# Kernel optimization log

Hardware: AMD Instinct MI355X
Metric: run time of the kernel (lower is better)

## Reference

```python
import jax, jax.numpy as jnp
import numpy as np

T = 8192
F = 128   # feature_size
H = 2048  # hidden_size
PRED_LEN = 12  # pred_length (fc_out head exists in module but is unused in forward)


def setup_inputs() -> dict:
    key = jax.random.key(0)
    ks = jax.random.split(key, 10)
    s_ih = 1.0 / np.sqrt(H)
    inp = {
        "x": jax.random.normal(ks[0], (T, F), dtype=jnp.float32),
        # PyTorch nn.LSTM params, gate order [i, f, g, o]
        "W_ih": jax.random.uniform(ks[1], (4 * H, F), jnp.float32, -s_ih, s_ih),
        "W_hh": jax.random.uniform(ks[2], (4 * H, H), jnp.float32, -s_ih, s_ih),
        "b_ih": jax.random.uniform(ks[3], (4 * H,), jnp.float32, -s_ih, s_ih),
        "b_hh": jax.random.uniform(ks[4], (4 * H,), jnp.float32, -s_ih, s_ih),
        # self.linear: Linear(H, H)
        "W_lin": jax.random.uniform(ks[5], (H, H), jnp.float32, -s_ih, s_ih),
        "b_lin": jax.random.uniform(ks[6], (H,), jnp.float32, -s_ih, s_ih),
        # self.one_out: Linear(H, 2)
        "W_out": jax.random.uniform(ks[7], (2, H), jnp.float32, -s_ih, s_ih),
        "b_out": jax.random.uniform(ks[8], (2,), jnp.float32, -s_ih, s_ih),
    }
    return inp


def _lstm_last_h(x, W_ih, W_hh, b_ih, b_hh):
    # x: [T, F]; returns final hidden state h: [H]
    # Precompute input projections for all timesteps: [T, 4H]
    x_proj = x @ W_ih.T + (b_ih + b_hh)

    def step(carry, xp):
        h, c = carry
        gates = xp + h @ W_hh.T  # [4H]
        i = jax.nn.sigmoid(gates[0 * H:1 * H])
        f = jax.nn.sigmoid(gates[1 * H:2 * H])
        g = jnp.tanh(gates[2 * H:3 * H])
        o = jax.nn.sigmoid(gates[3 * H:4 * H])
        c = f * c + i * g
        h = o * jnp.tanh(c)
        return (h, c), None

    h0 = jnp.zeros((H,), x.dtype)
    c0 = jnp.zeros((H,), x.dtype)
    (h, _), _ = jax.lax.scan(step, (h0, c0), x_proj)
    return h


def reference(x, W_ih, W_hh, b_ih, b_hh, W_lin, b_lin, W_out, b_out):
    h = _lstm_last_h(x, W_ih, W_hh, b_ih, b_hh)        # [H]
    y = h @ W_lin.T + b_lin                            # [H]
    y = y @ W_out.T + b_out                            # [2]
    return y.reshape(1, 1, 2)                          # matches torch (1,1,2)
```

## Files before the change

### kernel.cpp

```cpp
#include <hip/hip_runtime.h>


#define H      2048
#define TSTEPS 8192
#define FEAT   128
#define NBLK   256
#define NTHR   512

typedef float vf4 __attribute__((ext_vector_type(4)));
typedef float vf2 __attribute__((ext_vector_type(2)));
typedef unsigned long long u64;
typedef unsigned int u32;

__device__ __forceinline__ float sigm(float xv) {
  return __builtin_amdgcn_rcpf(1.0f + __expf(-xv));
}
__device__ __forceinline__ float tanh_(float xv) {
  return 1.0f - 2.0f * __builtin_amdgcn_rcpf(__expf(2.0f * xv) + 1.0f);
}

__device__ __forceinline__ u64 aload64(const u64* p) {
  return __hip_atomic_load(p, __ATOMIC_RELAXED, __HIP_MEMORY_SCOPE_AGENT);
}
__device__ __forceinline__ u32 aload32(const u32* p) {
  return __hip_atomic_load(p, __ATOMIC_RELAXED, __HIP_MEMORY_SCOPE_AGENT);
}
__device__ __forceinline__ void astoreu(u32* p, u32 v) {
  __hip_atomic_store(p, v, __ATOMIC_RELAXED, __HIP_MEMORY_SCOPE_AGENT);
}
__device__ __forceinline__ void astore64(u64* p, u64 v) {
  __hip_atomic_store(p, v, __ATOMIC_RELAXED, __HIP_MEMORY_SCOPE_AGENT);
}
__device__ __forceinline__ int  tag_of(u64 d) { return (int)(u32)(d >> 32); }
__device__ __forceinline__ float val_of(u64 d) { return __uint_as_float((u32)d); }
__device__ __forceinline__ u64  pack(int tag, float v) {
  return ((u64)(u32)tag << 32) | (u64)__float_as_uint(v);
}

#define DECLG(g) vf4 w##g##_0, w##g##_1, w##g##_2, w##g##_3, \
                     w##g##_4, w##g##_5, w##g##_6, w##g##_7; \
                 vf2 wih##g; float bias##g; float acc##g;

#define LOADG(g) { \
  const int row_ = (g) * H + j; \
  const float* wr_ = W_hh + (long)row_ * H; \
  w##g##_0 = *(const vf4*)(wr_ + 4*(ln      )); \
  w##g##_1 = *(const vf4*)(wr_ + 4*(ln +  64)); \
  w##g##_2 = *(const vf4*)(wr_ + 4*(ln + 128)); \
  w##g##_3 = *(const vf4*)(wr_ + 4*(ln + 192)); \
  w##g##_4 = *(const vf4*)(wr_ + 4*(ln + 256)); \
  w##g##_5 = *(const vf4*)(wr_ + 4*(ln + 320)); \
  w##g##_6 = *(const vf4*)(wr_ + 4*(ln + 384)); \
  w##g##_7 = *(const vf4*)(wr_ + 4*(ln + 448)); \
  wih##g  = *(const vf2*)(W_ih + (long)row_ * FEAT + 2*ln); \
  bias##g = b_ih[row_] + b_hh[row_]; }

#define PIN(g) asm volatile("" : \
  "+v"(w##g##_0), "+v"(w##g##_1), "+v"(w##g##_2), "+v"(w##g##_3), \
  "+v"(w##g##_4), "+v"(w##g##_5), "+v"(w##g##_6), "+v"(w##g##_7), \
  "+v"(wih##g), "+v"(bias##g));

#define LDSREAD(k, ldsrow) \
  const vf4 hv##k = *(const vf4*)&(ldsrow)[4*(ln + 64*(k))];

#define FMA_G(g, c) \
  acc##g = __builtin_fmaf(w##g##_##c.x, h4_.x, acc##g); \
  acc##g = __builtin_fmaf(w##g##_##c.y, h4_.y, acc##g); \
  acc##g = __builtin_fmaf(w##g##_##c.z, h4_.z, acc##g); \
  acc##g = __builtin_fmaf(w##g##_##c.w, h4_.w, acc##g);

#define FMA_C(c) { const vf4 h4_ = hv##c; \
  FMA_G(0, c) FMA_G(1, c) FMA_G(2, c) FMA_G(3, c) }

#define REDUCE(g) { float a_ = acc##g; \
  a_ += __shfl_xor(a_, 1);  a_ += __shfl_xor(a_, 2);  a_ += __shfl_xor(a_, 4); \
  a_ += __shfl_xor(a_, 8);  a_ += __shfl_xor(a_, 16); a_ += __shfl_xor(a_, 32); \
  acc##g = a_ + bias##g; }

__device__ __forceinline__ void poll_and_stage(const u32* __restrict__ slots,
                                               const u64* __restrict__ hq_par,
                                               int tgt,
                                               float* __restrict__ ldsrow,
                                               int wv, int ln) {
  const int base = wv * 256 + 4 * ln;
  const u64* hp = hq_par + base;
  u64 d0 = aload64(hp + 0);
  u64 d1 = aload64(hp + 1);
  u64 d2 = aload64(hp + 2);
  u64 d3 = aload64(hp + 3);

  const u32* sp = slots + wv * 32 + (ln & 31);
  const bool act = (ln < 32);
  int v0 = act ? (int)aload32(sp) : 0x7fffffff;
  int v1 = act ? (int)aload32(sp) : 0x7fffffff;
  int v2 = act ? (int)aload32(sp) : 0x7fffffff;
  while (!__all(v0 >= tgt)) {
    __builtin_amdgcn_s_sleep(1);
    v0 = v1;
    v1 = v2;
    v2 = (act && v1 < tgt) ? (int)aload32(sp) : v1;
  }
  while (!__all((tag_of(d0) >= tgt) & (tag_of(d1) >= tgt) &
                (tag_of(d2) >= tgt) & (tag_of(d3) >= tgt))) {
    if (tag_of(d0) < tgt) d0 = aload64(hp + 0);
    if (tag_of(d1) < tgt) d1 = aload64(hp + 1);
    if (tag_of(d2) < tgt) d2 = aload64(hp + 2);
    if (tag_of(d3) < tgt) d3 = aload64(hp + 3);
  }
  vf4 hv;
  hv.x = val_of(d0);
  hv.y = val_of(d1);
  hv.z = val_of(d2);
  hv.w = val_of(d3);
  *(vf4*)&ldsrow[base] = hv;
}

__global__ __launch_bounds__(NTHR, 2)
void lstm_persist(const float* __restrict__ x,
                  const float* __restrict__ W_ih,
                  const float* __restrict__ W_hh,
                  const float* __restrict__ b_ih,
                  const float* __restrict__ b_hh,
                  const float* __restrict__ W_lin,
                  const float* __restrict__ b_lin,
                  const float* __restrict__ W_out,
                  const float* __restrict__ b_out,
                  float* __restrict__ out,
                  float* __restrict__ ws)
{
  const int tid = threadIdx.x;
  const int b   = blockIdx.x;
  const int wv  = tid >> 6;
  const int ln  = tid & 63;

  u64* hq    = (u64*)ws;
  u32* slots = (u32*)(ws + 4 * H);

  __shared__ __align__(16) float h_lds[2][H];

  *(vf4*)&h_lds[0][4 * tid] = (vf4)(0.0f);

  const int j = b * 8 + wv;
  DECLG(0) DECLG(1) DECLG(2) DECLG(3)
  LOADG(0) LOADG(1) LOADG(2) LOADG(3)
  PIN(0) PIN(1) PIN(2) PIN(3)

  __syncthreads();

  float cst = 0.0f;

  #pragma unroll 1
  for (int t = 0; t < TSTEPS; ++t) {
    const vf2 xr = *(const vf2*)(x + (long)t * FEAT + 2 * ln);
    float* ldsrow = h_lds[t & 1];

    if (t > 0)
      poll_and_stage(slots, hq + (t & 1) * H, t, ldsrow, wv, ln);
    __syncthreads();

    LDSREAD(0, ldsrow) LDSREAD(1, ldsrow) LDSREAD(2, ldsrow) LDSREAD(3, ldsrow)
    LDSREAD(4, ldsrow) LDSREAD(5, ldsrow) LDSREAD(6, ldsrow) LDSREAD(7, ldsrow)

    acc0 = wih0.x * xr.x + wih0.y * xr.y;
    acc1 = wih1.x * xr.x + wih1.y * xr.y;
    acc2 = wih2.x * xr.x + wih2.y * xr.y;
    acc3 = wih3.x * xr.x + wih3.y * xr.y;

    FMA_C(0) FMA_C(1) FMA_C(2) FMA_C(3)
    FMA_C(4) FMA_C(5) FMA_C(6) FMA_C(7)

    REDUCE(0) REDUCE(1) REDUCE(2) REDUCE(3)

    const float iv = sigm(acc0);
    const float fv = sigm(acc1);
    const float gv = tanh_(acc2);
    const float ov = sigm(acc3);
    cst = fv * cst + iv * gv;
    const float hval = ov * tanh_(cst);

    if (ln == 0)
      astore64(hq + ((t + 1) & 1) * H + j, pack(t + 1, hval));
    __syncthreads();
    if (tid == 0)
      astoreu(slots + b, (u32)(t + 1));
  }

  {
    float* ldsrow = h_lds[0];
    poll_and_stage(slots, hq, TSTEPS, ldsrow, wv, ln);
    __syncthreads();

    float a0 = 0.0f;
    const float* wl = W_lin + (long)j * H;
    #pragma unroll
    for (int k = 0; k < 8; ++k) {
      const vf4 h4 = *(const vf4*)&ldsrow[4 * (ln + 64 * k)];
      const vf4 u  = *(const vf4*)(wl + 4 * (ln + 64 * k));
      a0 += u.x * h4.x + u.y * h4.y + u.z * h4.z + u.w * h4.w;
    }
    a0 += __shfl_xor(a0, 1);  a0 += __shfl_xor(a0, 2);  a0 += __shfl_xor(a0, 4);
    a0 += __shfl_xor(a0, 8);  a0 += __shfl_xor(a0, 16); a0 += __shfl_xor(a0, 32);

    if (ln == 0)
      astore64(hq + H + j, pack(TSTEPS + 1, a0 + b_lin[j]));
    __syncthreads();
    if (tid == 0)
      astoreu(slots + b, (u32)(TSTEPS + 1));
  }

  if (b == 0 && wv == 0) {
    const u32* sp = slots + 4 * ln;
    int v0 = (int)aload32(sp + 0), v1 = (int)aload32(sp + 1);
    int v2 = (int)aload32(sp + 2), v3 = (int)aload32(sp + 3);
    const int tgt = TSTEPS + 1;
    while (!__all((v0 >= tgt) & (v1 >= tgt) & (v2 >= tgt) & (v3 >= tgt))) {
      __builtin_amdgcn_s_sleep(1);
      if (v0 < tgt) v0 = (int)aload32(sp + 0);
      if (v1 < tgt) v1 = (int)aload32(sp + 1);
      if (v2 < tgt) v2 = (int)aload32(sp + 2);
      if (v3 < tgt) v3 = (int)aload32(sp + 3);
    }
    float p0 = 0.0f, p1 = 0.0f;
    #pragma unroll
    for (int k = 0; k < 32; ++k) {
      const u64 d  = aload64(hq + H + ln + 64 * k);
      const float y = val_of(d);
      const int c  = ln + 64 * k;
      p0 = __builtin_fmaf(W_out[c],     y, p0);
      p1 = __builtin_fmaf(W_out[H + c], y, p1);
    }
    p0 += __shfl_xor(p0, 1);  p0 += __shfl_xor(p0, 2);  p0 += __shfl_xor(p0, 4);
    p0 += __shfl_xor(p0, 8);  p0 += __shfl_xor(p0, 16); p0 += __shfl_xor(p0, 32);
    p1 += __shfl_xor(p1, 1);  p1 += __shfl_xor(p1, 2);  p1 += __shfl_xor(p1, 4);
    p1 += __shfl_xor(p1, 8);  p1 += __shfl_xor(p1, 16); p1 += __shfl_xor(p1, 32);
    if (ln == 0) {
      out[0] = p0 + b_out[0];
      out[1] = p1 + b_out[1];
    }
  }
}

extern "C" void kernel_launch(void* const* d_in, const int* in_sizes, int n_in,
                              void* d_out, int out_size, void* d_ws, size_t ws_size,
                              hipStream_t stream) {
  const float* x     = (const float*)d_in[0];
  const float* W_ih  = (const float*)d_in[1];
  const float* W_hh  = (const float*)d_in[2];
  const float* b_ih  = (const float*)d_in[3];
  const float* b_hh  = (const float*)d_in[4];
  const float* W_lin = (const float*)d_in[5];
  const float* b_lin = (const float*)d_in[6];
  const float* W_out = (const float*)d_in[7];
  const float* b_out = (const float*)d_in[8];

  lstm_persist<<<dim3(NBLK), dim3(NTHR), 0, stream>>>(
      x, W_ih, W_hh, b_ih, b_hh, W_lin, b_lin, W_out, b_out,
      (float*)d_out, (float*)d_ws);
}
```

Measured before the change: 30.03 ms.

## Inline polling with prefetched tags and LDS counter replacing end-of-step barrier

Replaces the per-step poll_and_stage call with an inline loop. The loop issues the tagged h loads and slot loads up front, pipelines the slot polling, and then re-polls only the stale tagged entries. The __syncthreads before publishing the block slot is removed. Instead, each wave increments an LDS counter after draining its stores, and the last wave to arrive publishes the slot. The aim is to cut barrier and polling latency on the serial recurrence critical path, at the cost of more subtle memory-ordering reasoning.

```diff
diff --git a/kernel.cpp b/kernel.cpp
--- a/kernel.cpp
+++ b/kernel.cpp
@@ -137,8 +137,10 @@
   u32* slots = (u32*)(ws + 4 * H);
 
   __shared__ __align__(16) float h_lds[2][H];
+  __shared__ int pub_cnt;
 
   *(vf4*)&h_lds[0][4 * tid] = (vf4)(0.0f);
+  if (tid == 0) pub_cnt = 0;
 
   const int j = b * 8 + wv;
   DECLG(0) DECLG(1) DECLG(2) DECLG(3)
@@ -151,11 +153,44 @@
 
   #pragma unroll 1
   for (int t = 0; t < TSTEPS; ++t) {
-    const vf2 xr = *(const vf2*)(x + (long)t * FEAT + 2 * ln);
     float* ldsrow = h_lds[t & 1];
-
-    if (t > 0)
-      poll_and_stage(slots, hq + (t & 1) * H, t, ldsrow, wv, ln);
+    vf2 xr;
+
+    if (t > 0) {
+      const int base = wv * 256 + 4 * ln;
+      const u64* hp = hq + (t & 1) * H + base;
+      u64 d0 = aload64(hp + 0);
+      u64 d1 = aload64(hp + 1);
+      u64 d2 = aload64(hp + 2);
+      u64 d3 = aload64(hp + 3);
+      const u32* sp = slots + wv * 32 + (ln & 31);
+      const bool act = (ln < 32);
+      int v0 = act ? (int)aload32(sp) : 0x7fffffff;
+      int v1 = act ? (int)aload32(sp) : 0x7fffffff;
+      int v2 = act ? (int)aload32(sp) : 0x7fffffff;
+      xr = *(const vf2*)(x + (long)t * FEAT + 2 * ln);
+      while (!__all(v0 >= t)) {
+        __builtin_amdgcn_s_sleep(1);
+        v0 = v1;
+        v1 = v2;
+        v2 = (act && v1 < t) ? (int)aload32(sp) : v1;
+      }
+      while (!__all((tag_of(d0) >= t) & (tag_of(d1) >= t) &
+                    (tag_of(d2) >= t) & (tag_of(d3) >= t))) {
+        if (tag_of(d0) < t) d0 = aload64(hp + 0);
+        if (tag_of(d1) < t) d1 = aload64(hp + 1);
+        if (tag_of(d2) < t) d2 = aload64(hp + 2);
+        if (tag_of(d3) < t) d3 = aload64(hp + 3);
+      }
+      vf4 hv;
+      hv.x = val_of(d0);
+      hv.y = val_of(d1);
+      hv.z = val_of(d2);
+      hv.w = val_of(d3);
+      *(vf4*)&ldsrow[base] = hv;
+    } else {
+      xr = *(const vf2*)(x + 2 * ln);
+    }
     __syncthreads();
 
     LDSREAD(0, ldsrow) LDSREAD(1, ldsrow) LDSREAD(2, ldsrow) LDSREAD(3, ldsrow)
@@ -180,9 +215,12 @@
 
     if (ln == 0)
       astore64(hq + ((t + 1) & 1) * H + j, pack(t + 1, hval));
-    __syncthreads();
-    if (tid == 0)
-      astoreu(slots + b, (u32)(t + 1));
+    asm volatile("s_waitcnt vmcnt(0)" ::: "memory");
+    if (ln == 0) {
+      const int old = atomicAdd(&pub_cnt, 1);
+      if (old == 8 * t + 7)
+        astoreu(slots + b, (u32)(t + 1));
+    }
   }
 
   {
```

New measurement: 67.90 ms. 2.26x slower.
